# Kernel optimization log

Hardware: AMD Instinct MI355X
Metric: run time of the kernel (lower is better)

## Reference

```python
import jax, jax.numpy as jnp
import numpy as np

B, V, C, A = 32, 48, 24, 6
NC, D, H, OUT = 10000, 128, 128, 167


def setup_inputs() -> dict:
    key = jax.random.key(0)
    ks = jax.random.split(key, 12)
    seqs = jax.random.randint(ks[0], (B, V, C), 0, NC + 1)
    ancestors = jax.random.randint(ks[1], (B, V, C, A), 0, NC + 1)
    length = jax.random.randint(ks[2], (B,), 1, V + 1)
    amask = (jax.random.uniform(ks[3], (B, V, C, A)) < 0.7).astype(jnp.float32)
    amask = amask.at[..., 0].set(1.0)  # first ancestor always valid
    emb = jax.random.normal(ks[4], (NC + 1, D), dtype=jnp.float32) * 0.02
    emb = emb.at[NC].set(0.0)  # padding row is zeros
    w_basic = jax.random.normal(ks[5], (D, 2 * D), dtype=jnp.float32) * (1.0 / np.sqrt(2 * D))
    u_basic_w = jax.random.normal(ks[6], (1, D), dtype=jnp.float32) * (1.0 / np.sqrt(D))
    u_basic_b = jnp.zeros((1,), jnp.float32)
    gru_wih = jax.random.normal(ks[7], (3 * H, D), dtype=jnp.float32) * (1.0 / np.sqrt(H))
    gru_whh = jax.random.normal(ks[8], (3 * H, H), dtype=jnp.float32) * (1.0 / np.sqrt(H))
    gru_bih = jnp.zeros((3 * H,), jnp.float32)
    gru_bhh = jnp.zeros((3 * H,), jnp.float32)
    out_w = jax.random.normal(ks[9], (OUT, H), dtype=jnp.float32) * (1.0 / np.sqrt(H))
    out_b = jnp.zeros((OUT,), jnp.float32)
    return dict(seqs=seqs, ancestors=ancestors, length=length, ancestor_length=amask,
                emb=emb, w_basic=w_basic, u_basic_w=u_basic_w, u_basic_b=u_basic_b,
                gru_wih=gru_wih, gru_whh=gru_whh, gru_bih=gru_bih, gru_bhh=gru_bhh,
                out_w=out_w, out_b=out_b)


def _gram_forward(seqs, ancestors, length, ancestor_length, emb, w_basic,
                  u_basic_w, u_basic_b, gru_wih, gru_whh, gru_bih, gru_bhh,
                  out_w, out_b):
    # gather embeddings
    seqs_e = emb[seqs]            # [B,V,C,D]
    anc_e = emb[ancestors]        # [B,V,C,A,D]
    seqs_rep = jnp.broadcast_to(seqs_e[..., None, :], anc_e.shape)
    # Bahdanau attention: mask applied to concat BEFORE the linear (as in source)
    cat = jnp.concatenate([seqs_rep, anc_e], axis=-1) * ancestor_length[..., None]  # [B,V,C,A,2D]
    hdd = jnp.tanh(jnp.einsum('bvcad,ed->bvcae', cat, w_basic))  # [B,V,C,A,D]
    score = jnp.einsum('bvcad,od->bvcao', hdd, u_basic_w) + u_basic_b  # [B,V,C,A,1]
    # mask_softmax over ancestor axis, faithful to the source (sum==0 -> -1)
    e = jnp.exp(score) * ancestor_length[..., None]
    s = jnp.sum(e, axis=3, keepdims=True)
    s = jnp.where(s == 0, -1.0, s)
    attn = e / s                  # [B,V,C,A,1]
    ctx = jnp.sum(attn * anc_e, axis=3)            # [B,V,C,D] weighted ancestor sum
    x = jnp.tanh(jnp.sum(ctx, axis=2))             # [B,V,D] visit embedding

    # single-layer GRU over visits (valid steps form a prefix, padded tail masked below)
    hsz = gru_whh.shape[1]
    def step(hstate, xt):
        gi = xt @ gru_wih.T + gru_bih              # [B,3H]
        gh = hstate @ gru_whh.T + gru_bhh
        ir, iz, inn = jnp.split(gi, 3, axis=-1)
        hr, hz, hn = jnp.split(gh, 3, axis=-1)
        r = jax.nn.sigmoid(ir + hr)
        z = jax.nn.sigmoid(iz + hz)
        n = jnp.tanh(inn + r * hn)
        hnew = (1.0 - z) * n + z * hstate
        return hnew, hnew
    h0 = jnp.zeros((x.shape[0], hsz), x.dtype)
    _, outs = jax.lax.scan(step, h0, jnp.swapaxes(x, 0, 1))  # [V,B,H]
    outs = jnp.swapaxes(outs, 0, 1)                          # [B,V,H]

    visit_mask = (jnp.arange(x.shape[1])[None, :] < length[:, None]).astype(x.dtype)
    context = jnp.einsum('bv,bvh->bh', visit_mask, outs)     # masked sum over visits
    logit = jax.nn.sigmoid(context @ out_w.T + out_b)        # dropout=eval (identity)
    return logit


def reference(seqs, ancestors, length, ancestor_length, emb, w_basic, u_basic_w,
              u_basic_b, gru_wih, gru_whh, gru_bih, gru_bhh, out_w, out_b):
    return _gram_forward(seqs, ancestors, length, ancestor_length, emb, w_basic,
                         u_basic_w, u_basic_b, gru_wih, gru_whh, gru_bih, gru_bhh,
                         out_w, out_b)
```

## Files before the change

### kernel.cpp

```cpp
#include <hip/hip_runtime.h>

#define BB 32
#define VV 48
#define CC 24
#define AA 6
#define NCODES 10001
#define DD 128
#define HH 128
#define OUTN 167
#define G3 384

typedef float f32x4 __attribute__((ext_vector_type(4)));

__device__ __forceinline__ float fast_tanh(float x) {
    return 1.0f - 2.0f / (1.0f + __expf(2.0f * x));
}
__device__ __forceinline__ float fast_sigmoid(float x) {
    return 1.0f / (1.0f + __expf(-x));
}
__device__ __forceinline__ float dot4(float4 a, float4 b) {
    return a.x * b.x + a.y * b.y + a.z * b.z + a.w * b.w;
}
__device__ __forceinline__ float dot4v(f32x4 a, f32x4 b) {
    return a.x * b.x + a.y * b.y + a.z * b.z + a.w * b.w;
}

__global__ __launch_bounds__(256) void k_precompute(
    const float* __restrict__ emb, const float* __restrict__ w_basic,
    float* __restrict__ P1, float* __restrict__ P2, int nrows)
{
    __shared__ float embs[8][128];
    int row0 = blockIdx.x * 8;
    int t = threadIdx.x;
    for (int i = t; i < 8 * 128; i += 256) {
        int r = i >> 7, d = i & 127;
        int row = row0 + r;
        embs[r][d] = (row < nrows) ? emb[row * 128 + d] : 0.0f;
    }
    __syncthreads();
    int e = t & 127, sel = t >> 7;
    const float* wrow = w_basic + e * 256 + sel * 128;
    float acc[8] = {0, 0, 0, 0, 0, 0, 0, 0};
#pragma unroll 8
    for (int d = 0; d < 128; ++d) {
        float w = wrow[d];
#pragma unroll
        for (int r = 0; r < 8; ++r) acc[r] += embs[r][d] * w;
    }
    float* dst = sel ? P2 : P1;
#pragma unroll
    for (int r = 0; r < 8; ++r) {
        int row = row0 + r;
        if (row < nrows) dst[row * 128 + e] = acc[r];
    }
}

__global__ __launch_bounds__(256) void k_attention(
    const int* __restrict__ seqs, const int* __restrict__ ancestors,
    const float* __restrict__ amask, const float* __restrict__ emb,
    const float* __restrict__ P1, const float* __restrict__ P2,
    const float* __restrict__ u_w, const float* __restrict__ u_b,
    float* __restrict__ x_out)
{
    __shared__ __align__(16) float u_s[128];
    __shared__ float sc_s[144];
    __shared__ float m_s[144];
    __shared__ int   anc_s[144];
    __shared__ float attn_s[144];
    __shared__ float sum_s[24];
    __shared__ float xred[256];
    int bv = blockIdx.x;
    int t = threadIdx.x;
    if (t < 128) u_s[t] = u_w[t];
    __syncthreads();
    float ub = u_b[0];
    int g = t >> 2, l = t & 3;
    for (int p = g; p < CC * AA; p += 64) {
        int c = p / AA, a = p - c * AA;
        int sidx = bv * CC + c;
        int s_code = seqs[sidx];
        int aidx = sidx * AA + a;
        int anc = ancestors[aidx];
        float m = amask[aidx];
        const float4* p14 = (const float4*)(P1 + s_code * 128);
        const float4* p24 = (const float4*)(P2 + anc * 128);
        const float4* u4 = (const float4*)u_s;
        float partial = 0.0f;
        int e4 = l * 8;
#pragma unroll 2
        for (int j = 0; j < 8; ++j) {
            float4 av = p14[e4 + j];
            float4 bv_ = p24[e4 + j];
            float4 uv = u4[e4 + j];
            partial += fast_tanh(m * (av.x + bv_.x)) * uv.x;
            partial += fast_tanh(m * (av.y + bv_.y)) * uv.y;
            partial += fast_tanh(m * (av.z + bv_.z)) * uv.z;
            partial += fast_tanh(m * (av.w + bv_.w)) * uv.w;
        }
        partial += __shfl_xor(partial, 1);
        partial += __shfl_xor(partial, 2);
        if (l == 0) {
            sc_s[p] = partial + ub;
            m_s[p] = m;
            anc_s[p] = anc;
        }
    }
    __syncthreads();
    if (t < CC * AA) attn_s[t] = __expf(sc_s[t]) * m_s[t];
    __syncthreads();
    if (t < CC) {
        float s = 0.0f;
#pragma unroll
        for (int a = 0; a < AA; ++a) s += attn_s[t * AA + a];
        sum_s[t] = (s == 0.0f) ? -1.0f : s;
    }
    __syncthreads();
    if (t < CC * AA) attn_s[t] = attn_s[t] / sum_s[t / AA];
    __syncthreads();
    int e = t & 127, hc = t >> 7;
    float acc = 0.0f;
    for (int c = hc * 12; c < hc * 12 + 12; ++c) {
#pragma unroll
        for (int a = 0; a < AA; ++a) {
            int p = c * AA + a;
            acc += attn_s[p] * emb[anc_s[p] * 128 + e];
        }
    }
    xred[t] = acc;
    __syncthreads();
    if (t < 128) {
        x_out[bv * 128 + t] = fast_tanh(xred[t] + xred[t + 128]);
    }
}

__global__ __launch_bounds__(384, 2) void k_gi(
    const float* __restrict__ x, const float* __restrict__ wih,
    const float* __restrict__ bih, float* __restrict__ gi)
{
    __shared__ __align__(16) float xs[8][128];
    int row0 = blockIdx.x * 8;
    int t = threadIdx.x;
    for (int i = t; i < 8 * 32; i += 384) {
        ((float4*)xs)[i] = ((const float4*)x)[row0 * 32 + i];
    }
    __syncthreads();
    const float4* wrow4 = (const float4*)(wih + t * 128);
    float acc[8] = {0, 0, 0, 0, 0, 0, 0, 0};
#pragma unroll 2
    for (int d4 = 0; d4 < 32; ++d4) {
        float4 wv = wrow4[d4];
#pragma unroll
        for (int r = 0; r < 8; ++r) {
            float4 xv = ((const float4*)xs[r])[d4];
            acc[r] += dot4(xv, wv);
        }
    }
    float bb = bih[t];
#pragma unroll
    for (int r = 0; r < 8; ++r) gi[(row0 + r) * G3 + t] = acc[r] + bb;
}

#define GL4(dst, base, OFF) \
    asm volatile("global_load_dwordx4 %0, %1, off offset:" #OFF \
                 : "=v"(dst) : "v"(base))

__global__ __launch_bounds__(256, 1) void k_gru(
    const float* __restrict__ gi, const float* __restrict__ whh,
    const float* __restrict__ bhh, const int* __restrict__ length,
    const float* __restrict__ out_w, const float* __restrict__ out_b,
    float* __restrict__ out)
{
    __shared__ __align__(16) float hs[2][128];
    __shared__ __align__(16) float ctxs[128];
    int b = blockIdx.x;
    int t = threadIdx.x;
    int o = t >> 1, half = t & 1;

    const f32x4* bwr = (const f32x4*)(whh + o * 128 + half * 64);
    const f32x4* bwz = (const f32x4*)(whh + (128 + o) * 128 + half * 64);
    const f32x4* bwn = (const f32x4*)(whh + (256 + o) * 128 + half * 64);

    f32x4 wr0, wr1, wr2, wr3, wr4, wr5, wr6, wr7,
          wr8, wr9, wr10, wr11, wr12, wr13, wr14, wr15;
    f32x4 wz0, wz1, wz2, wz3, wz4, wz5, wz6, wz7,
          wz8, wz9, wz10, wz11, wz12, wz13, wz14, wz15;
    f32x4 wn0, wn1, wn2, wn3, wn4, wn5, wn6, wn7,
          wn8, wn9, wn10, wn11, wn12, wn13, wn14, wn15;

    GL4(wr0,  bwr, 0);   GL4(wr1,  bwr, 16);  GL4(wr2,  bwr, 32);  GL4(wr3,  bwr, 48);
    GL4(wr4,  bwr, 64);  GL4(wr5,  bwr, 80);  GL4(wr6,  bwr, 96);  GL4(wr7,  bwr, 112);
    GL4(wr8,  bwr, 128); GL4(wr9,  bwr, 144); GL4(wr10, bwr, 160); GL4(wr11, bwr, 176);
    GL4(wr12, bwr, 192); GL4(wr13, bwr, 208); GL4(wr14, bwr, 224); GL4(wr15, bwr, 240);
    GL4(wz0,  bwz, 0);   GL4(wz1,  bwz, 16);  GL4(wz2,  bwz, 32);  GL4(wz3,  bwz, 48);
    GL4(wz4,  bwz, 64);  GL4(wz5,  bwz, 80);  GL4(wz6,  bwz, 96);  GL4(wz7,  bwz, 112);
    GL4(wz8,  bwz, 128); GL4(wz9,  bwz, 144); GL4(wz10, bwz, 160); GL4(wz11, bwz, 176);
    GL4(wz12, bwz, 192); GL4(wz13, bwz, 208); GL4(wz14, bwz, 224); GL4(wz15, bwz, 240);
    GL4(wn0,  bwn, 0);   GL4(wn1,  bwn, 16);  GL4(wn2,  bwn, 32);  GL4(wn3,  bwn, 48);
    GL4(wn4,  bwn, 64);  GL4(wn5,  bwn, 80);  GL4(wn6,  bwn, 96);  GL4(wn7,  bwn, 112);
    GL4(wn8,  bwn, 128); GL4(wn9,  bwn, 144); GL4(wn10, bwn, 160); GL4(wn11, bwn, 176);
    GL4(wn12, bwn, 192); GL4(wn13, bwn, 208); GL4(wn14, bwn, 224); GL4(wn15, bwn, 240);

    float bhr = 0.f, bhz = 0.f, bhn = 0.f;
    if (half == 0) {
        bhr = bhh[o];
        bhz = bhh[128 + o];
        bhn = bhh[256 + o];
    }
    if (t < 128) hs[0][t] = 0.0f;
    int len = length[b];
    float ctx = 0.0f;

    const float* gib = gi + b * VV * G3;
    float aR = 0.f, aZ = 0.f, aN = 0.f;
    float pR = 0.f, pZ = 0.f, pN = 0.f;
    if (half == 0) {
        aR = gib[o];       aZ = gib[128 + o];       aN = gib[256 + o];
        const float* g1 = gib + G3;
        pR = g1[o];        pZ = g1[128 + o];        pN = g1[256 + o];
    }
    asm volatile("s_waitcnt vmcnt(0)" ::: "memory");
    __builtin_amdgcn_sched_barrier(0);
    __syncthreads();

#define STEP2(J, A, B_) do {                                          \
        f32x4 hA = h4[J]; f32x4 hB = h4[J + 1];                       \
        ar0 += dot4v(wr##A, hA);  ar1 += dot4v(wr##B_, hB);           \
        az0 += dot4v(wz##A, hA);  az1 += dot4v(wz##B_, hB);           \
        an0 += dot4v(wn##A, hA);  an1 += dot4v(wn##B_, hB);           \
    } while (0)

    int cur = 0;
    for (int v = 0; v < VV; ++v) {
        float nR = 0.f, nZ = 0.f, nN = 0.f;
        if (half == 0 && v + 2 < VV) {
            const float* g = gib + (v + 2) * G3;
            nR = g[o]; nZ = g[128 + o]; nN = g[256 + o];
        }
        const f32x4* h4 = ((const f32x4*)hs[cur]) + half * 16;
        float ar0 = 0.f, ar1 = 0.f, az0 = 0.f, az1 = 0.f, an0 = 0.f, an1 = 0.f;
        STEP2(0, 0, 1);   STEP2(2, 2, 3);   STEP2(4, 4, 5);   STEP2(6, 6, 7);
        STEP2(8, 8, 9);   STEP2(10, 10, 11); STEP2(12, 12, 13); STEP2(14, 14, 15);
        float ar = ar0 + ar1;
        float az = az0 + az1;
        float an = an0 + an1;
        ar += __shfl_xor(ar, 1);
        az += __shfl_xor(az, 1);
        an += __shfl_xor(an, 1);
        if (half == 0) {
            float r = fast_sigmoid(aR + ar + bhr);
            float z = fast_sigmoid(aZ + az + bhz);
            float n = fast_tanh(aN + r * (an + bhn));
            float hold = hs[cur][o];
            float hnew = (1.0f - z) * n + z * hold;
            hs[cur ^ 1][o] = hnew;
            if (v < len) ctx += hnew;
        }
        aR = pR; aZ = pZ; aN = pN;
        pR = nR; pZ = nZ; pN = nN;
        cur ^= 1;
        __syncthreads();
    }
#undef STEP2

    if (half == 0) ctxs[o] = ctx;
    __syncthreads();
    if (t < OUTN) {
        const float4* w4 = (const float4*)(out_w + t * 128);
        const float4* c4 = (const float4*)ctxs;
        float a0 = 0.f, a1 = 0.f;
#pragma unroll 2
        for (int j = 0; j < 32; j += 2) {
            a0 += dot4(w4[j], c4[j]);
            a1 += dot4(w4[j + 1], c4[j + 1]);
        }
        out[b * OUTN + t] = fast_sigmoid(a0 + a1 + out_b[t]);
    }
}

extern "C" void kernel_launch(void* const* d_in, const int* in_sizes, int n_in,
                              void* d_out, int out_size, void* d_ws, size_t ws_size,
                              hipStream_t stream) {
    const int*   seqs      = (const int*)d_in[0];
    const int*   ancestors = (const int*)d_in[1];
    const int*   length    = (const int*)d_in[2];
    const float* amask     = (const float*)d_in[3];
    const float* emb       = (const float*)d_in[4];
    const float* w_basic   = (const float*)d_in[5];
    const float* u_w       = (const float*)d_in[6];
    const float* u_b       = (const float*)d_in[7];
    const float* wih       = (const float*)d_in[8];
    const float* whh       = (const float*)d_in[9];
    const float* bih       = (const float*)d_in[10];
    const float* bhh       = (const float*)d_in[11];
    const float* out_w     = (const float*)d_in[12];
    const float* out_b     = (const float*)d_in[13];
    float* out = (float*)d_out;

    float* ws = (float*)d_ws;
    float* P1 = ws;
    float* P2 = P1 + NCODES * 128;
    float* x  = P2 + NCODES * 128;
    float* gi = x + BB * VV * 128;

    k_precompute<<<(NCODES + 7) / 8, 256, 0, stream>>>(emb, w_basic, P1, P2, NCODES);
    k_attention<<<BB * VV, 256, 0, stream>>>(seqs, ancestors, amask, emb, P1, P2, u_w, u_b, x);
    k_gi<<<(BB * VV) / 8, 384, 0, stream>>>(x, wih, bih, gi);
    k_gru<<<BB, 256, 0, stream>>>(gi, whh, bhh, length, out_w, out_b, out);
}
```

Measured before the change: 136.1 us.

## Drop LDS staging in precompute/gi and stage GRU input gates in LDS

k_precompute no longer stages embedding rows in shared memory. It now reads emb and w_basic directly as float4, with each thread computing both P1 and P2 for 8 rows over 16-row blocks. k_gi reads x directly from global memory without the LDS copy and barrier. k_gru bulk-loads the precomputed input gates for 24 timesteps into LDS at once, reloading at step 24, in place of per-step register prefetch from global. This trades barrier and LDS costs for more redundant global/cache traffic, and adds a mid-loop bulk load stall in the recurrent kernel.

```diff
diff --git a/kernel.cpp b/kernel.cpp
--- a/kernel.cpp
+++ b/kernel.cpp
@@ -29,29 +29,33 @@
     const float* __restrict__ emb, const float* __restrict__ w_basic,
     float* __restrict__ P1, float* __restrict__ P2, int nrows)
 {
-    __shared__ float embs[8][128];
-    int row0 = blockIdx.x * 8;
+    int row0 = blockIdx.x * 16;
     int t = threadIdx.x;
-    for (int i = t; i < 8 * 128; i += 256) {
-        int r = i >> 7, d = i & 127;
-        int row = row0 + r;
-        embs[r][d] = (row < nrows) ? emb[row * 128 + d] : 0.0f;
-    }
-    __syncthreads();
-    int e = t & 127, sel = t >> 7;
-    const float* wrow = w_basic + e * 256 + sel * 128;
-    float acc[8] = {0, 0, 0, 0, 0, 0, 0, 0};
-#pragma unroll 8
-    for (int d = 0; d < 128; ++d) {
-        float w = wrow[d];
-#pragma unroll
-        for (int r = 0; r < 8; ++r) acc[r] += embs[r][d] * w;
-    }
-    float* dst = sel ? P2 : P1;
+    int tc = t & 127, grp = t >> 7;
+    int rbase = row0 + grp * 8;
+    const float4* w4 = (const float4*)w_basic;
+    const float4* e4 = (const float4*)emb;
+    float a0[8] = {}, a1[8] = {};
+#pragma unroll 2
+    for (int d4 = 0; d4 < 32; ++d4) {
+        float4 wv0 = w4[tc * 64 + d4];
+        float4 wv1 = w4[tc * 64 + 32 + d4];
+#pragma unroll
+        for (int r = 0; r < 8; ++r) {
+            int row = rbase + r;
+            if (row >= nrows) row = nrows - 1;
+            float4 ev = e4[row * 32 + d4];
+            a0[r] += dot4(ev, wv0);
+            a1[r] += dot4(ev, wv1);
+        }
+    }
 #pragma unroll
     for (int r = 0; r < 8; ++r) {
-        int row = row0 + r;
-        if (row < nrows) dst[row * 128 + e] = acc[r];
+        int row = rbase + r;
+        if (row < nrows) {
+            P1[row * 128 + tc] = a0[r];
+            P2[row * 128 + tc] = a1[r];
+        }
     }
 }
 
@@ -133,26 +137,21 @@
     }
 }
 
-__global__ __launch_bounds__(384, 2) void k_gi(
+__global__ __launch_bounds__(384) void k_gi(
     const float* __restrict__ x, const float* __restrict__ wih,
     const float* __restrict__ bih, float* __restrict__ gi)
 {
-    __shared__ __align__(16) float xs[8][128];
     int row0 = blockIdx.x * 8;
     int t = threadIdx.x;
-    for (int i = t; i < 8 * 32; i += 384) {
-        ((float4*)xs)[i] = ((const float4*)x)[row0 * 32 + i];
-    }
-    __syncthreads();
-    const float4* wrow4 = (const float4*)(wih + t * 128);
-    float acc[8] = {0, 0, 0, 0, 0, 0, 0, 0};
+    const float4* w4 = (const float4*)(wih + t * 128);
+    const float4* x4 = (const float4*)(x + row0 * 128);
+    float acc[8] = {};
 #pragma unroll 2
     for (int d4 = 0; d4 < 32; ++d4) {
-        float4 wv = wrow4[d4];
+        float4 wv = w4[d4];
 #pragma unroll
         for (int r = 0; r < 8; ++r) {
-            float4 xv = ((const float4*)xs[r])[d4];
-            acc[r] += dot4(xv, wv);
+            acc[r] += dot4(x4[r * 32 + d4], wv);
         }
     }
     float bb = bih[t];
@@ -170,6 +169,7 @@
     const float* __restrict__ out_w, const float* __restrict__ out_b,
     float* __restrict__ out)
 {
+    __shared__ __align__(16) float gl[24 * G3];
     __shared__ __align__(16) float hs[2][128];
     __shared__ __align__(16) float ctxs[128];
     int b = blockIdx.x;
@@ -200,6 +200,13 @@
     GL4(wn8,  bwn, 128); GL4(wn9,  bwn, 144); GL4(wn10, bwn, 160); GL4(wn11, bwn, 176);
     GL4(wn12, bwn, 192); GL4(wn13, bwn, 208); GL4(wn14, bwn, 224); GL4(wn15, bwn, 240);
 
+    const float4* gib4 = (const float4*)(gi + b * VV * G3);
+    {
+        float4* dst = (float4*)gl;
+#pragma unroll
+        for (int i = 0; i < 9; ++i) dst[t + i * 256] = gib4[t + i * 256];
+    }
+
     float bhr = 0.f, bhz = 0.f, bhn = 0.f;
     if (half == 0) {
         bhr = bhh[o];
@@ -210,14 +217,6 @@
     int len = length[b];
     float ctx = 0.0f;
 
-    const float* gib = gi + b * VV * G3;
-    float aR = 0.f, aZ = 0.f, aN = 0.f;
-    float pR = 0.f, pZ = 0.f, pN = 0.f;
-    if (half == 0) {
-        aR = gib[o];       aZ = gib[128 + o];       aN = gib[256 + o];
-        const float* g1 = gib + G3;
-        pR = g1[o];        pZ = g1[128 + o];        pN = g1[256 + o];
-    }
     asm volatile("s_waitcnt vmcnt(0)" ::: "memory");
     __builtin_amdgcn_sched_barrier(0);
     __syncthreads();
@@ -231,14 +230,22 @@
 
     int cur = 0;
     for (int v = 0; v < VV; ++v) {
-        float nR = 0.f, nZ = 0.f, nN = 0.f;
-        if (half == 0 && v + 2 < VV) {
-            const float* g = gib + (v + 2) * G3;
-            nR = g[o]; nZ = g[128 + o]; nN = g[256 + o];
+        if (v == 24) {
+            float4* dst = (float4*)gl;
+            const float4* src = gib4 + 2304;
+#pragma unroll
+            for (int i = 0; i < 9; ++i) dst[t + i * 256] = src[t + i * 256];
+            __syncthreads();
+        }
+        int vv = (v >= 24) ? (v - 24) : v;
+        float gir = 0.f, giz = 0.f, gin = 0.f;
+        if (half == 0) {
+            const float* g = gl + vv * G3;
+            gir = g[o]; giz = g[128 + o]; gin = g[256 + o];
         }
         const f32x4* h4 = ((const f32x4*)hs[cur]) + half * 16;
         float ar0 = 0.f, ar1 = 0.f, az0 = 0.f, az1 = 0.f, an0 = 0.f, an1 = 0.f;
-        STEP2(0, 0, 1);   STEP2(2, 2, 3);   STEP2(4, 4, 5);   STEP2(6, 6, 7);
+        STEP2(0, 0, 1);   STEP2(2, 2, 3);    STEP2(4, 4, 5);    STEP2(6, 6, 7);
         STEP2(8, 8, 9);   STEP2(10, 10, 11); STEP2(12, 12, 13); STEP2(14, 14, 15);
         float ar = ar0 + ar1;
         float az = az0 + az1;
@@ -247,16 +254,14 @@
         az += __shfl_xor(az, 1);
         an += __shfl_xor(an, 1);
         if (half == 0) {
-            float r = fast_sigmoid(aR + ar + bhr);
-            float z = fast_sigmoid(aZ + az + bhz);
-            float n = fast_tanh(aN + r * (an + bhn));
+            float r = fast_sigmoid(gir + ar + bhr);
+            float z = fast_sigmoid(giz + az + bhz);
+            float n = fast_tanh(gin + r * (an + bhn));
             float hold = hs[cur][o];
             float hnew = (1.0f - z) * n + z * hold;
             hs[cur ^ 1][o] = hnew;
             if (v < len) ctx += hnew;
         }
-        aR = pR; aZ = pZ; aN = pN;
-        pR = nR; pZ = nZ; pN = nN;
         cur ^= 1;
         __syncthreads();
     }
@@ -302,7 +307,7 @@
     float* x  = P2 + NCODES * 128;
     float* gi = x + BB * VV * 128;
 
-    k_precompute<<<(NCODES + 7) / 8, 256, 0, stream>>>(emb, w_basic, P1, P2, NCODES);
+    k_precompute<<<(NCODES + 15) / 16, 256, 0, stream>>>(emb, w_basic, P1, P2, NCODES);
     k_attention<<<BB * VV, 256, 0, stream>>>(seqs, ancestors, amask, emb, P1, P2, u_w, u_b, x);
     k_gi<<<(BB * VV) / 8, 384, 0, stream>>>(x, wih, bih, gi);
     k_gru<<<BB, 256, 0, stream>>>(gi, whh, bhh, length, out_w, out_b, out);
```

After: 164.3 us. 20.7% more time.
